# Kernel tuning notes

Hardware: AMD Instinct MI355X
Metric: run time of the kernel (lower is better)

Reference implementation:

```python
import jax, jax.numpy as jnp
import numpy as np

N, A, H, W = 8, 3, 336, 336
IMG_W, IMG_H = 1333.0, 800.0
PRE_TOP_K = 2000
POST_NMS_TOP_N = 1000
NMS_THR = 0.7
MIN_SIZE = 0.0
TO_REMOVE = 1.0
XFORM_CLIP = float(np.log(1000.0 / 16.0))
NEG = -1e9


def setup_inputs() -> dict:
    key = jax.random.key(0)
    k1, k2, k3, k4, k5, k6 = jax.random.split(key, 6)
    M = A * H * W
    x1 = jax.random.uniform(k1, (N, M)) * (IMG_W - 1.0)
    y1 = jax.random.uniform(k2, (N, M)) * (IMG_H - 1.0)
    bw = jax.random.uniform(k3, (N, M)) * 256.0 + 4.0
    bh = jax.random.uniform(k4, (N, M)) * 256.0 + 4.0
    anchors = jnp.stack([x1, y1, x1 + bw, y1 + bh], axis=-1).astype(jnp.float32)
    logits = jax.random.normal(k5, (N, A, H, W), dtype=jnp.float32)
    bbox_reg = jax.random.normal(k6, (N, A * 4, H, W), dtype=jnp.float32) * 0.25
    return {"anchors": anchors, "logits": logits, "bbox_reg": bbox_reg}


def _decode(anchors, deltas):
    # anchors, deltas: [..., 4] in xyxy / (dx,dy,dw,dh)
    w = anchors[..., 2] - anchors[..., 0] + TO_REMOVE
    h = anchors[..., 3] - anchors[..., 1] + TO_REMOVE
    cx = anchors[..., 0] + 0.5 * w
    cy = anchors[..., 1] + 0.5 * h
    dx, dy, dw, dh = deltas[..., 0], deltas[..., 1], deltas[..., 2], deltas[..., 3]
    dw = jnp.minimum(dw, XFORM_CLIP)
    dh = jnp.minimum(dh, XFORM_CLIP)
    pcx = dx * w + cx
    pcy = dy * h + cy
    pw = jnp.exp(dw) * w
    ph = jnp.exp(dh) * h
    return jnp.stack([pcx - 0.5 * pw, pcy - 0.5 * ph,
                      pcx + 0.5 * pw - 1.0, pcy + 0.5 * ph - 1.0], axis=-1)


def _nms_single(boxes, scores):
    # boxes: [K,4], scores: [K] (invalid entries already set to NEG)
    areas = (boxes[:, 2] - boxes[:, 0] + TO_REMOVE) * (boxes[:, 3] - boxes[:, 1] + TO_REMOVE)

    def step(live, _):
        j = jnp.argmax(live)
        sj = live[j]
        bj = boxes[j]
        xx1 = jnp.maximum(bj[0], boxes[:, 0])
        yy1 = jnp.maximum(bj[1], boxes[:, 1])
        xx2 = jnp.minimum(bj[2], boxes[:, 2])
        yy2 = jnp.minimum(bj[3], boxes[:, 3])
        inter = jnp.maximum(xx2 - xx1 + TO_REMOVE, 0.0) * jnp.maximum(yy2 - yy1 + TO_REMOVE, 0.0)
        iou = inter / (areas[j] + areas - inter)
        live = jnp.where(iou > NMS_THR, NEG, live)
        live = live.at[j].set(NEG)
        valid = sj > NEG * 0.5
        return live, (jnp.where(valid, bj, 0.0), jnp.where(valid, sj, 0.0))

    _, (sel_boxes, sel_scores) = jax.lax.scan(step, scores, None, length=POST_NMS_TOP_N)
    return sel_boxes, sel_scores


def _forward(anchors, logits, bbox_reg):
    n, a, h, w = logits.shape
    # objectness scores: [N, A*H*W], ordered as (H, W, A) like the torch permute
    scores = jax.nn.sigmoid(jnp.transpose(logits, (0, 2, 3, 1)).reshape(n, -1))
    reg = bbox_reg.reshape(n, a, 4, h, w)
    reg = jnp.transpose(reg, (0, 3, 4, 1, 2)).reshape(n, -1, 4)
    k = min(scores.shape[1], PRE_TOP_K)
    top_scores, idx = jax.lax.top_k(scores, k)  # sorted descending
    reg_k = jnp.take_along_axis(reg, idx[..., None], axis=1)
    anc_k = jnp.take_along_axis(anchors, idx[..., None], axis=1)
    props = _decode(anc_k, reg_k)
    x1 = jnp.clip(props[..., 0], 0.0, IMG_W - 1.0)
    y1 = jnp.clip(props[..., 1], 0.0, IMG_H - 1.0)
    x2 = jnp.clip(props[..., 2], 0.0, IMG_W - 1.0)
    y2 = jnp.clip(props[..., 3], 0.0, IMG_H - 1.0)
    clipped = jnp.stack([x1, y1, x2, y2], axis=-1)
    ws = x2 - x1 + TO_REMOVE
    hs = y2 - y1 + TO_REMOVE
    keep = (ws >= MIN_SIZE) & (hs >= MIN_SIZE)
    sc = jnp.where(keep, top_scores, NEG)
    sel_boxes, sel_scores = jax.vmap(_nms_single)(clipped, sc)
    # [N, POST_NMS_TOP_N, 5] = boxes + score
    return jnp.concatenate([sel_boxes, sel_scores[..., None]], axis=-1)


def reference(anchors, logits, bbox_reg):
    return _forward(anchors, logits, bbox_reg)
```

## Files before the change

### kernel.cpp

```cpp
#include <hip/hip_runtime.h>
#include <stdint.h>

#define N_BATCH 8
#define A_ 3
#define H_ 336
#define W_ 336
#define HW_ (H_*W_)
#define M_ (A_*HW_)
#define K_TOP 2000
#define POST_N 1000
#define NMS_THR_ 0.7f
#define NEG_ (-1e9f)
#define VALID_THR_ (-5e8f)
#define CAND_CAP 4096
#define NBINS 4096
#define BIN_SHIFT 20
#define HBLK 32
#define SEG_ (M_/HBLK)
#define XCLIP 4.135166556742356f

#define NPAD 2048
#define NW 32
#define NCHUNK 32
#define RING 4
#define RBLK 128

typedef unsigned long long u64;

__device__ __forceinline__ unsigned int flip_key(float x) {
    unsigned int u = __float_as_uint(x);
    return (u & 0x80000000u) ? ~u : (u | 0x80000000u);
}
__device__ __forceinline__ float unflip_key(unsigned int k) {
    unsigned int u = (k & 0x80000000u) ? (k & 0x7fffffffu) : ~k;
    return __uint_as_float(u);
}

__device__ __forceinline__ void gload_lds16(const u64* g, u64* l) {
    __builtin_amdgcn_global_load_lds(
        (const __attribute__((address_space(1))) unsigned int*)(const void*)g,
        (__attribute__((address_space(3))) unsigned int*)(void*)l,
        16, 0, 0);
}

__global__ __launch_bounds__(512) void k_hist(const float* __restrict__ logits,
                                              unsigned short* __restrict__ ghist,
                                              unsigned int* __restrict__ cnt) {
    __shared__ unsigned int h[2][NBINS];
    int n = blockIdx.y, b = blockIdx.x;
    if (b == 0 && threadIdx.x < 2) cnt[n * 2 + threadIdx.x] = 0;
    unsigned int* hf = &h[0][0];
    for (int i = threadIdx.x; i < 2 * NBINS; i += 512) hf[i] = 0;
    __syncthreads();
    int wp = (threadIdx.x >> 6) & 1;
    const float4* lp = (const float4*)(logits + (size_t)n * M_ + (size_t)b * SEG_);
    const int nq = SEG_ / 4;
    for (int q = threadIdx.x; q < nq; q += 512) {
        float4 v = lp[q];
        atomicAdd(&h[wp][flip_key(v.x) >> BIN_SHIFT], 1u);
        atomicAdd(&h[wp][flip_key(v.y) >> BIN_SHIFT], 1u);
        atomicAdd(&h[wp][flip_key(v.z) >> BIN_SHIFT], 1u);
        atomicAdd(&h[wp][flip_key(v.w) >> BIN_SHIFT], 1u);
    }
    __syncthreads();
    unsigned short* gp = ghist + ((size_t)n * HBLK + b) * NBINS;
    for (int i = threadIdx.x; i < NBINS; i += 512)
        gp[i] = (unsigned short)(h[0][i] + h[1][i]);
}

__global__ __launch_bounds__(512) void k_compact(const float* __restrict__ logits,
                                                 const unsigned short* __restrict__ ghist,
                                                 unsigned int* __restrict__ cnt,
                                                 u64* __restrict__ cand) {
    __shared__ unsigned int binsum[NBINS];
    __shared__ unsigned int part[512];
    __shared__ unsigned int scanb[512];
    __shared__ u64 bufHi[2048];
    __shared__ u64 bufLo[4096];
    __shared__ unsigned int lcntHi, lcntLo, gbaseHi, gbaseLo;
    __shared__ int Bsh;
    int n = blockIdx.y, b = blockIdx.x;
    int t = threadIdx.x;
    if (t == 0) { lcntHi = 0; lcntLo = 0; }
    const unsigned short* base = ghist + (size_t)n * HBLK * NBINS;
    for (int i = t; i < NBINS; i += 512) {
        unsigned int s = 0;
        #pragma unroll 8
        for (int sb = 0; sb < HBLK; ++sb) s += base[(size_t)sb * NBINS + i];
        binsum[i] = s;
    }
    __syncthreads();
    int hi = NBINS - 8 * t;
    int lo = hi - 8;
    unsigned int s = 0;
    for (int bb = lo; bb < hi; ++bb) s += binsum[bb];
    part[t] = s;
    scanb[t] = s;
    __syncthreads();
    for (int off = 1; off < 512; off <<= 1) {
        unsigned int v = scanb[t];
        unsigned int addv = (t >= off) ? scanb[t - off] : 0u;
        __syncthreads();
        scanb[t] = v + addv;
        __syncthreads();
    }
    unsigned int incl = scanb[t];
    unsigned int prefix = incl - part[t];
    if (prefix < K_TOP && incl >= K_TOP) {
        unsigned int acc = prefix;
        for (int bb = hi - 1; bb >= lo; --bb) {
            unsigned int c = binsum[bb];
            if (acc + c >= K_TOP) { Bsh = bb; break; }
            acc += c;
        }
    }
    __syncthreads();
    unsigned int B = (unsigned int)Bsh;
    const int qbase = b * SEG_;
    const float4* lp = (const float4*)(logits + (size_t)n * M_ + (size_t)qbase);
    const int nq = SEG_ / 4;
    for (int q = t; q < nq; q += 512) {
        float4 v = lp[q];
        float vv[4] = {v.x, v.y, v.z, v.w};
        #pragma unroll
        for (int e = 0; e < 4; ++e) {
            unsigned int u = flip_key(vv[e]);
            unsigned int bin = u >> BIN_SHIFT;
            if (bin >= B) {
                int qq = qbase + q * 4 + e;
                int a = qq / HW_;
                int hw = qq - a * HW_;
                unsigned int m = (unsigned int)(hw * A_ + a);
                u64 key = ((u64)u << 32) | (unsigned int)(~m);
                if (bin > B) {
                    unsigned int pos = atomicAdd(&lcntHi, 1u);
                    if (pos < 2048) bufHi[pos] = key;
                } else {
                    unsigned int pos = atomicAdd(&lcntLo, 1u);
                    if (pos < 4096) bufLo[pos] = key;
                }
            }
        }
    }
    __syncthreads();
    unsigned int Lhi = (lcntHi < 2048u) ? lcntHi : 2048u;
    unsigned int Llo = (lcntLo < 4096u) ? lcntLo : 4096u;
    if (t == 0) gbaseHi = atomicAdd(&cnt[n * 2], Lhi);
    if (t == 1) gbaseLo = atomicAdd(&cnt[n * 2 + 1], Llo);
    __syncthreads();
    u64* cp = cand + (size_t)n * CAND_CAP;
    for (unsigned int i = t; i < Lhi; i += 512)
        cp[gbaseHi + i] = bufHi[i];
    for (unsigned int i = t; i < Llo; i += 512) {
        unsigned int idx = CAND_CAP - 1u - (gbaseLo + i);
        if ((int)idx >= K_TOP) cp[idx] = bufLo[i];
    }
}

__global__ __launch_bounds__(512) void k_rank(const u64* __restrict__ cand,
                                              const unsigned int* __restrict__ cnt,
                                              const float* __restrict__ anchors,
                                              const float* __restrict__ breg,
                                              float4* __restrict__ boxes,
                                              float* __restrict__ scores,
                                              float* __restrict__ areas) {
    __shared__ u64 keys[CAND_CAP];
    __shared__ unsigned short psum[512];
    int n = blockIdx.y;
    int bx = blockIdx.x;
    unsigned int T = cnt[n * 2];
    unsigned int Lc = cnt[n * 2 + 1];
    unsigned int Ls = (Lc < (unsigned int)(CAND_CAP - K_TOP)) ? Lc : (unsigned int)(CAND_CAP - K_TOP);
    int loStart = CAND_CAP - (int)Ls;
    int p0 = bx * RBLK;
    if (p0 >= (int)T && p0 + RBLK <= loStart) return;
    const u64* cp = cand + (size_t)n * CAND_CAP;
    for (int i = threadIdx.x; i < (int)T; i += 512) keys[i] = cp[i];
    for (int i = loStart + threadIdx.x; i < CAND_CAP; i += 512) keys[i] = cp[i];
    __syncthreads();
    int t = threadIdx.x;
    int tq = t & 3;
    int cl = t >> 2;
    int ci = p0 + cl;
    bool isHi = (ci < (int)T);
    bool isLo = (!isHi) && (ci >= loStart) && (ci < CAND_CAP);
    unsigned int r = 0;
    u64 ki = 0;
    int jb = 0, je = 0;
    unsigned int radd = 0;
    if (isHi) { ki = keys[ci]; jb = 0; je = (int)T; }
    else if (isLo) { ki = keys[ci]; jb = loStart; je = CAND_CAP; radd = T; }
    int j = jb + tq;
    for (; j + 12 < je; j += 16) {
        r += (keys[j] > ki);
        r += (keys[j + 4] > ki);
        r += (keys[j + 8] > ki);
        r += (keys[j + 12] > ki);
    }
    for (; j < je; j += 4) r += (keys[j] > ki);
    psum[t] = (unsigned short)r;
    __syncthreads();
    if (tq == 0 && (isHi || isLo)) {
        unsigned int rank = radd + psum[t] + psum[t + 1] + psum[t + 2] + psum[t + 3];
        if (rank < K_TOP) {
            unsigned int u = (unsigned int)(ki >> 32);
            unsigned int m = ~((unsigned int)ki);
            float logit = unflip_key(u);
            int a = (int)(m % 3u);
            int hw = (int)(m / 3u);
            float4 anc = ((const float4*)anchors)[(size_t)n * M_ + m];
            size_t rb = ((size_t)n * 12 + a * 4) * HW_ + hw;
            float dx = breg[rb];
            float dy = breg[rb + (size_t)HW_];
            float dw = breg[rb + (size_t)2 * HW_];
            float dh = breg[rb + (size_t)3 * HW_];
            float score = 1.0f / (1.0f + expf(-logit));
            float w = anc.z - anc.x + 1.0f;
            float h = anc.w - anc.y + 1.0f;
            float cx = anc.x + 0.5f * w;
            float cy = anc.y + 0.5f * h;
            dw = fminf(dw, XCLIP);
            dh = fminf(dh, XCLIP);
            float pcx = dx * w + cx;
            float pcy = dy * h + cy;
            float pw = expf(dw) * w;
            float ph = expf(dh) * h;
            float x1 = pcx - 0.5f * pw;
            float y1 = pcy - 0.5f * ph;
            float x2 = pcx + 0.5f * pw - 1.0f;
            float y2 = pcy + 0.5f * ph - 1.0f;
            x1 = fminf(fmaxf(x1, 0.0f), 1332.0f);
            y1 = fminf(fmaxf(y1, 0.0f), 799.0f);
            x2 = fminf(fmaxf(x2, 0.0f), 1332.0f);
            y2 = fminf(fmaxf(y2, 0.0f), 799.0f);
            float ww = x2 - x1 + 1.0f;
            float hh = y2 - y1 + 1.0f;
            bool keep = (ww >= 0.0f) && (hh >= 0.0f);
            int g = n * K_TOP + (int)rank;
            boxes[g] = make_float4(x1, y1, x2, y2);
            scores[g] = keep ? score : NEG_;
            areas[g] = ww * hh;
        }
    }
}

#define JT 512
#define RT 64
__global__ __launch_bounds__(256) void k_edges(const float4* __restrict__ boxes,
                                               const float* __restrict__ areas,
                                               u64* __restrict__ adj) {
    int n = blockIdx.z;
    int by = blockIdx.y;
    int bx = blockIdx.x;
    if (by > bx * 8 + 7) return;
    __shared__ float4 jb[JT];
    __shared__ float ja[JT];
    int r0 = by * RT;
    int j0 = bx * JT;
    for (int j = threadIdx.x; j < JT; j += 256) {
        int jj = j0 + j;
        if (jj < K_TOP) {
            jb[j] = boxes[(size_t)n * K_TOP + jj];
            ja[j] = areas[(size_t)n * K_TOP + jj];
        } else {
            jb[j] = make_float4(-1e8f, -1e8f, -1e8f, -1e8f);
            ja[j] = 0.0f;
        }
    }
    __syncthreads();
    int i = r0 + (threadIdx.x >> 2);
    if (i >= K_TOP) return;
    float4 bi = boxes[(size_t)n * K_TOP + i];
    float ai = areas[(size_t)n * K_TOP + i];
    #pragma unroll
    for (int rep = 0; rep < 2; ++rep) {
        int wl = (threadIdx.x & 3) + rep * 4;
        u64 bits = 0;
        int base = wl * 64;
        #pragma unroll 8
        for (int b = 0; b < 64; ++b) {
            float4 bj = jb[base + b];
            float xx1 = fmaxf(bi.x, bj.x);
            float yy1 = fmaxf(bi.y, bj.y);
            float xx2 = fminf(bi.z, bj.z);
            float yy2 = fminf(bi.w, bj.w);
            float inter = fmaxf(xx2 - xx1 + 1.0f, 0.0f) * fmaxf(yy2 - yy1 + 1.0f, 0.0f);
            float iou = inter / (ai + ja[base + b] - inter);
            bits |= ((u64)(iou > NMS_THR_)) << b;
        }
        adj[((size_t)n * NPAD + i) * NW + (j0 >> 6) + wl] = bits;
    }
}

__global__ __launch_bounds__(256) void k_resolve(const float4* __restrict__ boxes,
                                                 const float* __restrict__ scores,
                                                 const u64* __restrict__ adj,
                                                 float* __restrict__ out) {
    __shared__ u64 ring[RING][64 * NW];
    __shared__ float sls[NPAD];
    __shared__ unsigned char alive[NPAD];
    __shared__ int ready[RING];
    __shared__ int progress;
    __shared__ unsigned int scanbuf[256];
    int n = blockIdx.x;
    int tid = threadIdx.x;
    int wave = tid >> 6, lane = tid & 63;
    const u64* ab = adj + (size_t)n * NPAD * NW;

    for (int i = tid; i < NPAD; i += 256) {
        sls[i] = (i < K_TOP) ? scores[(size_t)n * K_TOP + i] : NEG_;
        alive[i] = 0;
    }
    if (tid < RING) ready[tid] = 0;
    if (tid == 0) progress = 0;
    __syncthreads();

    if (wave == 0) {
        u64 supreg = 0;
        int survTot = 0;
        for (int c = 0; c < NCHUNK; ++c) {
            int slot = c & (RING - 1);
            while (__hip_atomic_load(&ready[slot], __ATOMIC_ACQUIRE,
                                     __HIP_MEMORY_SCOPE_WORKGROUP) != c + 1)
                __builtin_amdgcn_s_sleep(1);
            int k = lane;
            int gi = c * 64 + k;
            u64 colk = ring[slot][k * NW + c];
            u64 supc = __shfl(supreg, c, 64);
            bool validk = (sls[gi] > VALID_THR_) && !((supc >> k) & 1ull);
            u64 below = (k == 0) ? 0ull : ((1ull << k) - 1ull);
            u64 rel = colk & below;
            bool a = validk;
            u64 am = __ballot(a);
            while (true) {
                bool anew = validk && ((am & rel) == 0ull);
                u64 am2 = __ballot(anew);
                if (am2 == am) { a = anew; break; }
                am = am2;
            }
            alive[gi] = a ? 1 : 0;
            int nal = (int)__popcll(am);
            survTot += nal;
            if (survTot >= POST_N) {
                if (lane == 0)
                    __hip_atomic_store(&progress, NCHUNK, __ATOMIC_RELEASE,
                                       __HIP_MEMORY_SCOPE_WORKGROUP);
                break;
            }
            int w = lane & 31, half = lane >> 5;
            u64 acc = 0;
            u64 m = am & (half ? 0xAAAAAAAAAAAAAAAAull : 0x5555555555555555ull);
            while (m) {
                int kk[8];
                kk[0] = __ffsll((unsigned long long)m) - 1; m &= m - 1;
                #pragma unroll
                for (int e = 1; e < 8; ++e) {
                    kk[e] = m ? (__ffsll((unsigned long long)m) - 1) : kk[0];
                    if (m) m &= m - 1;
                }
                u64 r0 = ring[slot][kk[0] * NW + w];
                u64 r1 = ring[slot][kk[1] * NW + w];
                u64 r2 = ring[slot][kk[2] * NW + w];
                u64 r3 = ring[slot][kk[3] * NW + w];
                u64 r4 = ring[slot][kk[4] * NW + w];
                u64 r5 = ring[slot][kk[5] * NW + w];
                u64 r6 = ring[slot][kk[6] * NW + w];
                u64 r7 = ring[slot][kk[7] * NW + w];
                acc |= (r0 | r1) | (r2 | r3) | ((r4 | r5) | (r6 | r7));
            }
            acc |= __shfl_down(acc, 32);
            if (lane < 32) supreg |= acc;
            if (lane == 0)
                __hip_atomic_store(&progress, c + 1, __ATOMIC_RELEASE,
                                   __HIP_MEMORY_SCOPE_WORKGROUP);
        }
    } else {
        for (int c = wave - 1; c < NCHUNK; c += 3) {
            int slot = c & (RING - 1);
            int p;
            while ((p = __hip_atomic_load(&progress, __ATOMIC_ACQUIRE,
                                          __HIP_MEMORY_SCOPE_WORKGROUP)) < c - 3)
                __builtin_amdgcn_s_sleep(1);
            if (p >= NCHUNK) break;
            const u64* src = ab + (size_t)c * 64 * NW + lane * 2;
            u64* dst = &ring[slot][0];
            #pragma unroll
            for (int it = 0; it < 16; ++it)
                gload_lds16(src + (size_t)it * 128, dst + it * 128);
            __builtin_amdgcn_s_waitcnt(0);
            if (lane == 0)
                __hip_atomic_store(&ready[slot], c + 1, __ATOMIC_RELEASE,
                                   __HIP_MEMORY_SCOPE_WORKGROUP);
        }
    }
    __syncthreads();

    int i0 = tid * 8;
    unsigned int c2 = 0;
    for (int i = i0; i < i0 + 8; ++i) c2 += alive[i];
    scanbuf[tid] = c2;
    __syncthreads();
    for (int off = 1; off < 256; off <<= 1) {
        unsigned int v = scanbuf[tid];
        unsigned int addv = (tid >= off) ? scanbuf[tid - off] : 0u;
        __syncthreads();
        scanbuf[tid] = v + addv;
        __syncthreads();
    }
    unsigned int r = scanbuf[tid] - c2;
    unsigned int total = scanbuf[255];
    float* op = out + (size_t)n * POST_N * 5;
    const float4* bb = boxes + (size_t)n * K_TOP;
    for (int i = i0; i < i0 + 8; ++i) {
        if (alive[i]) {
            if (r < POST_N) {
                float4 b = bb[i];
                op[r * 5 + 0] = b.x;
                op[r * 5 + 1] = b.y;
                op[r * 5 + 2] = b.z;
                op[r * 5 + 3] = b.w;
                op[r * 5 + 4] = sls[i];
            }
            r++;
        }
    }
    unsigned int S = (total > POST_N) ? POST_N : total;
    for (unsigned int q = S + tid; q < POST_N; q += 256) {
        op[q * 5 + 0] = 0.0f;
        op[q * 5 + 1] = 0.0f;
        op[q * 5 + 2] = 0.0f;
        op[q * 5 + 3] = 0.0f;
        op[q * 5 + 4] = 0.0f;
    }
}

extern "C" void kernel_launch(void* const* d_in, const int* in_sizes, int n_in,
                              void* d_out, int out_size, void* d_ws, size_t ws_size,
                              hipStream_t stream) {
    const float* anchors = (const float*)d_in[0];
    const float* logits  = (const float*)d_in[1];
    const float* breg    = (const float*)d_in[2];
    float* out = (float*)d_out;
    char* ws = (char*)d_ws;

    unsigned int* cnt     = (unsigned int*)(ws);
    unsigned short* ghist = (unsigned short*)(ws + 128);
    u64* cand             = (u64*)(ws + 2097280);
    u64* adj              = (u64*)(ws + 128);
    float4* boxes         = (float4*)(ws + 4194432);
    float* scores         = (float*)(ws + 4450432);
    float* areas          = (float*)(ws + 4514432);

    k_hist<<<dim3(HBLK, 8), 512, 0, stream>>>(logits, ghist, cnt);
    k_compact<<<dim3(HBLK, 8), 512, 0, stream>>>(logits, ghist, cnt, cand);
    k_rank<<<dim3(CAND_CAP / RBLK, 8), 512, 0, stream>>>(cand, cnt, anchors, breg,
                                                         boxes, scores, areas);
    k_edges<<<dim3(NPAD / JT, NPAD / RT, 8), 256, 0, stream>>>(boxes, areas, adj);
    k_resolve<<<8, 256, 0, stream>>>(boxes, scores, adj, out);
}
```

Before: 196.6 us.

## Widen histogram privatization, shuffle-scan threshold, and rank via wave-uniform global loads

The histogram kernel now spreads its LDS atomics over four private sub-histograms instead of two, cutting same-bin contention. The compact kernel sums bins in registers with vectorized 16-bit loads and finds the threshold bin with a wave shuffle scan, dropping the LDS binsum array and the block-wide scan with many barriers. The rank kernel no longer stages candidate keys in LDS. Each wave instead reads a wave-uniform slice of keys straight from global memory (scalar or broadcast loads) while each thread compares against its own key, and the four partial counts are summed afterwards. This removes the LDS fill and its barrier, but relies on cache hits for the repeated global reads.

Result: no change. 196.3 us (-0.1%).

```diff
diff --git a/kernel.cpp b/kernel.cpp
--- a/kernel.cpp
+++ b/kernel.cpp
@@ -46,13 +46,13 @@
 __global__ __launch_bounds__(512) void k_hist(const float* __restrict__ logits,
                                               unsigned short* __restrict__ ghist,
                                               unsigned int* __restrict__ cnt) {
-    __shared__ unsigned int h[2][NBINS];
+    __shared__ unsigned int h[4][NBINS];
     int n = blockIdx.y, b = blockIdx.x;
     if (b == 0 && threadIdx.x < 2) cnt[n * 2 + threadIdx.x] = 0;
     unsigned int* hf = &h[0][0];
-    for (int i = threadIdx.x; i < 2 * NBINS; i += 512) hf[i] = 0;
-    __syncthreads();
-    int wp = (threadIdx.x >> 6) & 1;
+    for (int i = threadIdx.x; i < 4 * NBINS; i += 512) hf[i] = 0;
+    __syncthreads();
+    int wp = (threadIdx.x >> 6) & 3;
     const float4* lp = (const float4*)(logits + (size_t)n * M_ + (size_t)b * SEG_);
     const int nq = SEG_ / 4;
     for (int q = threadIdx.x; q < nq; q += 512) {
@@ -65,16 +65,14 @@
     __syncthreads();
     unsigned short* gp = ghist + ((size_t)n * HBLK + b) * NBINS;
     for (int i = threadIdx.x; i < NBINS; i += 512)
-        gp[i] = (unsigned short)(h[0][i] + h[1][i]);
+        gp[i] = (unsigned short)(h[0][i] + h[1][i] + h[2][i] + h[3][i]);
 }
 
 __global__ __launch_bounds__(512) void k_compact(const float* __restrict__ logits,
                                                  const unsigned short* __restrict__ ghist,
                                                  unsigned int* __restrict__ cnt,
                                                  u64* __restrict__ cand) {
-    __shared__ unsigned int binsum[NBINS];
-    __shared__ unsigned int part[512];
-    __shared__ unsigned int scanb[512];
+    __shared__ unsigned int wsum[8];
     __shared__ u64 bufHi[2048];
     __shared__ u64 bufLo[4096];
     __shared__ unsigned int lcntHi, lcntLo, gbaseHi, gbaseLo;
@@ -83,36 +81,39 @@
     int t = threadIdx.x;
     if (t == 0) { lcntHi = 0; lcntLo = 0; }
     const unsigned short* base = ghist + (size_t)n * HBLK * NBINS;
-    for (int i = t; i < NBINS; i += 512) {
-        unsigned int s = 0;
-        #pragma unroll 8
-        for (int sb = 0; sb < HBLK; ++sb) s += base[(size_t)sb * NBINS + i];
-        binsum[i] = s;
-    }
-    __syncthreads();
-    int hi = NBINS - 8 * t;
-    int lo = hi - 8;
-    unsigned int s = 0;
-    for (int bb = lo; bb < hi; ++bb) s += binsum[bb];
-    part[t] = s;
-    scanb[t] = s;
-    __syncthreads();
-    for (int off = 1; off < 512; off <<= 1) {
-        unsigned int v = scanb[t];
-        unsigned int addv = (t >= off) ? scanb[t - off] : 0u;
-        __syncthreads();
-        scanb[t] = v + addv;
-        __syncthreads();
-    }
-    unsigned int incl = scanb[t];
-    unsigned int prefix = incl - part[t];
+    int tt = 511 - t;
+    unsigned int c0 = 0, c1 = 0, c2 = 0, c3 = 0, c4 = 0, c5 = 0, c6 = 0, c7 = 0;
+    #pragma unroll 8
+    for (int sb = 0; sb < HBLK; ++sb) {
+        uint4 v = *(const uint4*)(base + (size_t)sb * NBINS + 8 * tt);
+        c0 += v.x & 0xffffu; c1 += v.x >> 16;
+        c2 += v.y & 0xffffu; c3 += v.y >> 16;
+        c4 += v.z & 0xffffu; c5 += v.z >> 16;
+        c6 += v.w & 0xffffu; c7 += v.w >> 16;
+    }
+    unsigned int part = c0 + c1 + c2 + c3 + c4 + c5 + c6 + c7;
+    int wave = t >> 6, lane = t & 63;
+    unsigned int sc = part;
+    #pragma unroll
+    for (int off = 1; off < 64; off <<= 1) {
+        unsigned int v = __shfl_up(sc, off, 64);
+        if (lane >= off) sc += v;
+    }
+    if (lane == 63) wsum[wave] = sc;
+    __syncthreads();
+    unsigned int wpre = 0;
+    #pragma unroll
+    for (int wv = 0; wv < 8; ++wv) wpre += (wv < wave) ? wsum[wv] : 0u;
+    unsigned int incl = sc + wpre;
+    unsigned int prefix = incl - part;
     if (prefix < K_TOP && incl >= K_TOP) {
         unsigned int acc = prefix;
-        for (int bb = hi - 1; bb >= lo; --bb) {
-            unsigned int c = binsum[bb];
-            if (acc + c >= K_TOP) { Bsh = bb; break; }
-            acc += c;
-        }
+        int found = -1;
+        #define BSTEP(q, cq) if (found < 0) { if (acc + (cq) >= K_TOP) found = 8 * tt + (q); else acc += (cq); }
+        BSTEP(7, c7) BSTEP(6, c6) BSTEP(5, c5) BSTEP(4, c4)
+        BSTEP(3, c3) BSTEP(2, c2) BSTEP(1, c1) BSTEP(0, c0)
+        #undef BSTEP
+        Bsh = found;
     }
     __syncthreads();
     unsigned int B = (unsigned int)Bsh;
@@ -164,7 +165,6 @@
                                               float4* __restrict__ boxes,
                                               float* __restrict__ scores,
                                               float* __restrict__ areas) {
-    __shared__ u64 keys[CAND_CAP];
     __shared__ unsigned short psum[512];
     int n = blockIdx.y;
     int bx = blockIdx.x;
@@ -175,33 +175,55 @@
     int p0 = bx * RBLK;
     if (p0 >= (int)T && p0 + RBLK <= loStart) return;
     const u64* cp = cand + (size_t)n * CAND_CAP;
-    for (int i = threadIdx.x; i < (int)T; i += 512) keys[i] = cp[i];
-    for (int i = loStart + threadIdx.x; i < CAND_CAP; i += 512) keys[i] = cp[i];
-    __syncthreads();
     int t = threadIdx.x;
-    int tq = t & 3;
-    int cl = t >> 2;
+    int cl = t & (RBLK - 1);
+    int tq = t >> 7;
     int ci = p0 + cl;
     bool isHi = (ci < (int)T);
-    bool isLo = (!isHi) && (ci >= loStart) && (ci < CAND_CAP);
+    bool isLo = (!isHi) && (ci >= loStart);
+    u64 ki = (isHi || isLo) ? cp[ci] : 0ull;
     unsigned int r = 0;
-    u64 ki = 0;
-    int jb = 0, je = 0;
-    unsigned int radd = 0;
-    if (isHi) { ki = keys[ci]; jb = 0; je = (int)T; }
-    else if (isLo) { ki = keys[ci]; jb = loStart; je = CAND_CAP; radd = T; }
-    int j = jb + tq;
-    for (; j + 12 < je; j += 16) {
-        r += (keys[j] > ki);
-        r += (keys[j + 4] > ki);
-        r += (keys[j + 8] > ki);
-        r += (keys[j + 12] > ki);
-    }
-    for (; j < je; j += 4) r += (keys[j] > ki);
+    if (__any(isHi)) {
+        int len = (int)T;
+        int qlen = (len + 3) >> 2;
+        int j0 = tq * qlen;
+        int j1 = j0 + qlen; if (j1 > len) j1 = len;
+        j0 = __builtin_amdgcn_readfirstlane(j0);
+        j1 = __builtin_amdgcn_readfirstlane(j1);
+        unsigned int rh = 0;
+        int j = j0;
+        for (; j + 8 <= j1; j += 8) {
+            u64 k0 = cp[j],     k1 = cp[j + 1], k2 = cp[j + 2], k3 = cp[j + 3];
+            u64 k4 = cp[j + 4], k5 = cp[j + 5], k6 = cp[j + 6], k7 = cp[j + 7];
+            rh += (k0 > ki) + (k1 > ki) + (k2 > ki) + (k3 > ki);
+            rh += (k4 > ki) + (k5 > ki) + (k6 > ki) + (k7 > ki);
+        }
+        for (; j < j1; ++j) rh += (cp[j] > ki);
+        if (isHi) r = rh;
+    }
+    if (__any(isLo)) {
+        int len = CAND_CAP - loStart;
+        int qlen = (len + 3) >> 2;
+        int j0 = loStart + tq * qlen;
+        int j1 = j0 + qlen; if (j1 > CAND_CAP) j1 = CAND_CAP;
+        j0 = __builtin_amdgcn_readfirstlane(j0);
+        j1 = __builtin_amdgcn_readfirstlane(j1);
+        unsigned int rl = 0;
+        int j = j0;
+        for (; j + 8 <= j1; j += 8) {
+            u64 k0 = cp[j],     k1 = cp[j + 1], k2 = cp[j + 2], k3 = cp[j + 3];
+            u64 k4 = cp[j + 4], k5 = cp[j + 5], k6 = cp[j + 6], k7 = cp[j + 7];
+            rl += (k0 > ki) + (k1 > ki) + (k2 > ki) + (k3 > ki);
+            rl += (k4 > ki) + (k5 > ki) + (k6 > ki) + (k7 > ki);
+        }
+        for (; j < j1; ++j) rl += (cp[j] > ki);
+        if (isLo) r = rl;
+    }
     psum[t] = (unsigned short)r;
     __syncthreads();
-    if (tq == 0 && (isHi || isLo)) {
-        unsigned int rank = radd + psum[t] + psum[t + 1] + psum[t + 2] + psum[t + 3];
+    if (t < RBLK && (isHi || isLo)) {
+        unsigned int rank = (isLo ? T : 0u)
+                          + psum[t] + psum[t + 128] + psum[t + 256] + psum[t + 384];
         if (rank < K_TOP) {
             unsigned int u = (unsigned int)(ki >> 32);
             unsigned int m = ~((unsigned int)ki);
```
